# Kernel optimization log

Hardware: AMD Instinct MI355X
Metric: run time of the kernel (lower is better)

Reference implementation:

```python
import jax, jax.numpy as jnp
import numpy as np

HIDDEN = 1024
FFN = 4096
N_EXPERTS = 8
TOP_K = 2


def setup_inputs() -> dict:
    key = jax.random.key(0)
    ks = jax.random.split(key, 6)
    x = jax.random.normal(ks[0], (2, 2048, HIDDEN), dtype=jnp.float32)
    Wr = jax.random.normal(ks[1], (N_EXPERTS, HIDDEN), dtype=jnp.float32) * 0.02
    W1 = jax.random.normal(ks[2], (N_EXPERTS, FFN, HIDDEN), dtype=jnp.float32) * 0.02
    b1 = jnp.zeros((N_EXPERTS, FFN), dtype=jnp.float32)
    W2 = jax.random.normal(ks[3], (N_EXPERTS, HIDDEN, FFN), dtype=jnp.float32) * 0.02
    b2 = jnp.zeros((N_EXPERTS, HIDDEN), dtype=jnp.float32)
    return {"x": x, "Wr": Wr, "W1": W1, "b1": b1, "W2": W2, "b2": b2}


def reference(x, Wr, W1, b1, W2, b2):
    # x: [B, S, D]; Wr: [E, D]; W1: [E, F, D]; W2: [E, D, F]
    B, S, D = x.shape
    E = Wr.shape[0]
    xf = x.reshape(-1, D)                              # [T, D]
    T = xf.shape[0]
    logits = xf @ Wr.T                                 # [T, E]
    probs = jax.nn.softmax(logits, axis=-1)
    top_v, top_i = jax.lax.top_k(probs, TOP_K)         # [T, K]
    top_v = top_v / jnp.sum(top_v, axis=-1, keepdims=True)
    # combine weights: zero except the top-k experts per token
    comb = jnp.zeros((T, E), dtype=xf.dtype).at[jnp.arange(T)[:, None], top_i].add(top_v)
    # run every expert densely (same math as gather/FFN/weighted-scatter)
    h = jax.nn.gelu(jnp.einsum('td,efd->etf', xf, W1) + b1[:, None, :], approximate=False)  # [E, T, F]
    y = jnp.einsum('etf,edf->etd', h, W2) + b2[:, None, :]                                   # [E, T, D]
    out = jnp.einsum('etd,te->td', y, comb)            # weighted combine
    return out.reshape(B, S, D)
```

## Files before the change

kernel.cpp:

```cpp
#include <hip/hip_runtime.h>

#define HIDDEN 1024
#define FFN    4096
#define NEXP   8
#define TOKENS 4096
#define ASSIGN 8192

typedef __attribute__((ext_vector_type(8))) short s8v;
typedef __attribute__((ext_vector_type(4))) float f4v;

__device__ __forceinline__ float bf2f(ushort u) {
    return __uint_as_float(((unsigned int)u) << 16);
}
__device__ __forceinline__ ushort f2bf(float f) {
    unsigned int x = __float_as_uint(f);
    return (ushort)((x + 0x7fffu + ((x >> 16) & 1u)) >> 16);
}

#define GLDS16(g, l) __builtin_amdgcn_global_load_lds( \
    (const __attribute__((address_space(1))) unsigned int*)(g), \
    (__attribute__((address_space(3))) unsigned int*)(l), 16, 0, 0)

__global__ void conv_kernel(const float4* __restrict__ src, ushort4* __restrict__ dst) {
    const int i = blockIdx.x * blockDim.x + threadIdx.x;
    const float4 v = src[i];
    ushort4 o;
    o.x = f2bf(v.x); o.y = f2bf(v.y); o.z = f2bf(v.z); o.w = f2bf(v.w);
    dst[i] = o;
}

__global__ void router_kernel(const float* __restrict__ x, const float* __restrict__ Wr,
                              int* __restrict__ counts, int* __restrict__ topk_idx,
                              float* __restrict__ topk_w) {
    const int tok  = blockIdx.x;
    const int lane = threadIdx.x;
    float acc[NEXP];
#pragma unroll
    for (int e = 0; e < NEXP; ++e) acc[e] = 0.f;
#pragma unroll
    for (int i = 0; i < HIDDEN / 64; ++i) {
        const int idx = i * 64 + lane;
        const float xv = x[(size_t)tok * HIDDEN + idx];
#pragma unroll
        for (int e = 0; e < NEXP; ++e) acc[e] += xv * Wr[e * HIDDEN + idx];
    }
#pragma unroll
    for (int e = 0; e < NEXP; ++e) {
#pragma unroll
        for (int off = 32; off > 0; off >>= 1) acc[e] += __shfl_xor(acc[e], off);
    }
    if (lane == 0) {
        int i0 = 0;
        for (int e = 1; e < NEXP; ++e) if (acc[e] > acc[i0]) i0 = e;
        int i1 = (i0 == 0) ? 1 : 0;
        for (int e = 0; e < NEXP; ++e) if (e != i0 && acc[e] > acc[i1]) i1 = e;
        const float e1 = expf(acc[i1] - acc[i0]);
        const float s  = 1.f + e1;
        topk_idx[tok * 2 + 0] = i0;
        topk_idx[tok * 2 + 1] = i1;
        topk_w[tok * 2 + 0]   = 1.f / s;
        topk_w[tok * 2 + 1]   = e1 / s;
        atomicAdd(&counts[i0], 1);
        atomicAdd(&counts[i1], 1);
    }
}

__global__ void prefix_kernel(const int* __restrict__ counts, int* __restrict__ offsets,
                              int* __restrict__ cursors) {
    if (threadIdx.x == 0) {
        int s = 0;
        for (int e = 0; e < NEXP; ++e) { offsets[e] = s; cursors[e] = s; s += counts[e]; }
        offsets[NEXP] = s;
    }
}

__global__ void scatter_kernel(const int* __restrict__ topk_idx, const float* __restrict__ topk_w,
                               int* __restrict__ cursors, int* __restrict__ token_list,
                               float* __restrict__ weight_list, int* __restrict__ slot_of) {
    const int a = blockIdx.x * blockDim.x + threadIdx.x;
    if (a >= ASSIGN) return;
    const int e   = topk_idx[a];
    const int pos = atomicAdd(&cursors[e], 1);
    token_list[pos]  = a >> 1;
    weight_list[pos] = topk_w[a];
    slot_of[a]       = pos;
}

__global__ __launch_bounds__(256)
void gemm1_kernel(const ushort* __restrict__ x, const ushort* __restrict__ W1,
                  const float* __restrict__ b1, const int* __restrict__ token_list,
                  const int* __restrict__ counts, const int* __restrict__ offsets,
                  ushort* __restrict__ h) {
    const int e      = blockIdx.z;
    const int n_e    = counts[e];
    const int tile_m = blockIdx.y;
    if (n_e <= 0 || tile_m * 128 >= n_e) return;
    const int tile_n = blockIdx.x;
    const int base   = offsets[e];

    __shared__ __align__(16) ushort As[128 * 32];
    __shared__ __align__(16) ushort Bs[128 * 32];

    const int t    = threadIdx.x;
    const int lane = t & 63;
    const int wv   = t >> 6;
    const int srow = t >> 2;
    const int scol = (t & 3) * 8;

    const int r0 = tile_m * 128 + srow;
    const int r1 = r0 + 64;
    const int tokA0 = token_list[base + (r0 < n_e ? r0 : n_e - 1)];
    const int tokA1 = token_list[base + (r1 < n_e ? r1 : n_e - 1)];
    const ushort* gA0 = x + (size_t)tokA0 * HIDDEN + scol;
    const ushort* gA1 = x + (size_t)tokA1 * HIDDEN + scol;
    const ushort* gB0 = W1 + ((size_t)e * FFN + tile_n * 128 + srow) * HIDDEN + scol;
    const ushort* gB1 = W1 + ((size_t)e * FFN + tile_n * 128 + 64 + srow) * HIDDEN + scol;

    ushort* lA0 = As + wv * 512;
    ushort* lA1 = As + 2048 + wv * 512;
    ushort* lB0 = Bs + wv * 512;
    ushort* lB1 = Bs + 2048 + wv * 512;

    f4v acc[4][4];
#pragma unroll
    for (int i = 0; i < 4; ++i)
#pragma unroll
        for (int j = 0; j < 4; ++j) { f4v z = {0.f, 0.f, 0.f, 0.f}; acc[i][j] = z; }

    const int row_off = (wv & 1) * 64;
    const int col_off = (wv >> 1) * 64;
    const int l15 = lane & 15;
    const int lq  = lane >> 4;

    for (int k0 = 0; k0 < HIDDEN; k0 += 32) {
        GLDS16(gA0 + k0, lA0);
        GLDS16(gA1 + k0, lA1);
        GLDS16(gB0 + k0, lB0);
        GLDS16(gB1 + k0, lB1);
        __syncthreads();
        s8v a[4], b[4];
#pragma unroll
        for (int i = 0; i < 4; ++i) a[i] = *(const s8v*)(As + (row_off + i * 16 + l15) * 32 + lq * 8);
#pragma unroll
        for (int j = 0; j < 4; ++j) b[j] = *(const s8v*)(Bs + (col_off + j * 16 + l15) * 32 + lq * 8);
#pragma unroll
        for (int i = 0; i < 4; ++i)
#pragma unroll
            for (int j = 0; j < 4; ++j)
                acc[i][j] = __builtin_amdgcn_mfma_f32_16x16x32_bf16(a[i], b[j], acc[i][j], 0, 0, 0);
        __syncthreads();
    }

    const int mrem = n_e - tile_m * 128;
#pragma unroll
    for (int i = 0; i < 4; ++i) {
#pragma unroll
        for (int r = 0; r < 4; ++r) {
            const int m_loc = row_off + i * 16 + lq * 4 + r;
            if (m_loc < mrem) {
                const size_t hrow = (size_t)(base + tile_m * 128 + m_loc) * FFN;
#pragma unroll
                for (int j = 0; j < 4; ++j) {
                    const int colF = tile_n * 128 + col_off + j * 16 + l15;
                    float v = acc[i][j][r] + b1[e * FFN + colF];
                    v = 0.5f * v * (1.0f + erff(v * 0.70710678118654752f));
                    h[hrow + colF] = f2bf(v);
                }
            }
        }
    }
}

__global__ __launch_bounds__(256)
void gemm2_kernel(const ushort* __restrict__ h, const ushort* __restrict__ W2,
                  const float* __restrict__ b2, const float* __restrict__ weight_list,
                  const int* __restrict__ counts, const int* __restrict__ offsets,
                  ushort* __restrict__ y) {
    const int e      = blockIdx.z;
    const int n_e    = counts[e];
    const int tile_m = blockIdx.y;
    if (n_e <= 0 || tile_m * 128 >= n_e) return;
    const int tile_n = blockIdx.x;
    const int base   = offsets[e];

    __shared__ __align__(16) ushort As[128 * 32];
    __shared__ __align__(16) ushort Bs[128 * 32];

    const int t    = threadIdx.x;
    const int lane = t & 63;
    const int wv   = t >> 6;
    const int srow = t >> 2;
    const int scol = (t & 3) * 8;

    const int r0 = tile_m * 128 + srow;
    const int r1 = r0 + 64;
    const int slot0 = base + (r0 < n_e ? r0 : n_e - 1);
    const int slot1 = base + (r1 < n_e ? r1 : n_e - 1);
    const ushort* gA0 = h + (size_t)slot0 * FFN + scol;
    const ushort* gA1 = h + (size_t)slot1 * FFN + scol;
    const ushort* gB0 = W2 + ((size_t)e * HIDDEN + tile_n * 128 + srow) * FFN + scol;
    const ushort* gB1 = W2 + ((size_t)e * HIDDEN + tile_n * 128 + 64 + srow) * FFN + scol;

    ushort* lA0 = As + wv * 512;
    ushort* lA1 = As + 2048 + wv * 512;
    ushort* lB0 = Bs + wv * 512;
    ushort* lB1 = Bs + 2048 + wv * 512;

    f4v acc[4][4];
#pragma unroll
    for (int i = 0; i < 4; ++i)
#pragma unroll
        for (int j = 0; j < 4; ++j) { f4v z = {0.f, 0.f, 0.f, 0.f}; acc[i][j] = z; }

    const int row_off = (wv & 1) * 64;
    const int col_off = (wv >> 1) * 64;
    const int l15 = lane & 15;
    const int lq  = lane >> 4;

    for (int k0 = 0; k0 < FFN; k0 += 32) {
        GLDS16(gA0 + k0, lA0);
        GLDS16(gA1 + k0, lA1);
        GLDS16(gB0 + k0, lB0);
        GLDS16(gB1 + k0, lB1);
        __syncthreads();
        s8v a[4], b[4];
#pragma unroll
        for (int i = 0; i < 4; ++i) a[i] = *(const s8v*)(As + (row_off + i * 16 + l15) * 32 + lq * 8);
#pragma unroll
        for (int j = 0; j < 4; ++j) b[j] = *(const s8v*)(Bs + (col_off + j * 16 + l15) * 32 + lq * 8);
#pragma unroll
        for (int i = 0; i < 4; ++i)
#pragma unroll
            for (int j = 0; j < 4; ++j)
                acc[i][j] = __builtin_amdgcn_mfma_f32_16x16x32_bf16(a[i], b[j], acc[i][j], 0, 0, 0);
        __syncthreads();
    }

    const int mrem = n_e - tile_m * 128;
#pragma unroll
    for (int i = 0; i < 4; ++i) {
#pragma unroll
        for (int r = 0; r < 4; ++r) {
            const int m_loc = row_off + i * 16 + lq * 4 + r;
            if (m_loc < mrem) {
                const int slot = base + tile_m * 128 + m_loc;
                const float wgt = weight_list[slot];
#pragma unroll
                for (int j = 0; j < 4; ++j) {
                    const int colD = tile_n * 128 + col_off + j * 16 + l15;
                    const float v = acc[i][j][r] + b2[e * HIDDEN + colD];
                    y[(size_t)slot * HIDDEN + colD] = f2bf(v * wgt);
                }
            }
        }
    }
}

__global__ void combine_kernel(const int* __restrict__ slot_of, const ushort* __restrict__ y,
                               float* __restrict__ out) {
    const int idx = blockIdx.x * blockDim.x + threadIdx.x;
    const int t = idx >> 8;
    const int d = (idx & 255) * 4;
    const int s0 = slot_of[t * 2 + 0];
    const int s1 = slot_of[t * 2 + 1];
    const ushort4 a = *(const ushort4*)(y + (size_t)s0 * HIDDEN + d);
    const ushort4 b = *(const ushort4*)(y + (size_t)s1 * HIDDEN + d);
    float4 o;
    o.x = bf2f(a.x) + bf2f(b.x);
    o.y = bf2f(a.y) + bf2f(b.y);
    o.z = bf2f(a.z) + bf2f(b.z);
    o.w = bf2f(a.w) + bf2f(b.w);
    *(float4*)(out + (size_t)t * HIDDEN + d) = o;
}

extern "C" void kernel_launch(void* const* d_in, const int* in_sizes, int n_in,
                              void* d_out, int out_size, void* d_ws, size_t ws_size,
                              hipStream_t stream) {
    const float* x  = (const float*)d_in[0];
    const float* Wr = (const float*)d_in[1];
    const float* W1 = (const float*)d_in[2];
    const float* b1 = (const float*)d_in[3];
    const float* W2 = (const float*)d_in[4];
    const float* b2 = (const float*)d_in[5];
    float* out = (float*)d_out;

    char* ws = (char*)d_ws;
    int*    counts      = (int*)(ws + 0);
    int*    offsets     = (int*)(ws + 256);
    int*    cursors     = (int*)(ws + 512);
    int*    topk_idx    = (int*)(ws + 1024);
    float*  topk_w      = (float*)(ws + 1024 + 32768);
    int*    slot_of     = (int*)(ws + 1024 + 65536);
    int*    token_list  = (int*)(ws + 1024 + 98304);
    float*  weight_list = (float*)(ws + 1024 + 131072);
    ushort* x_bf        = (ushort*)(ws + (1 << 20));
    ushort* wbuf        = (ushort*)(ws + (1 << 20) + 8388608);
    ushort* h           = (ushort*)(ws + (1 << 20) + 8388608 + 67108864);
    ushort* y           = (ushort*)(ws + (1 << 20) + 8388608 + 2 * 67108864ull);

    const int NW = NEXP * FFN * HIDDEN;

    hipMemsetAsync(counts, 0, 64, stream);
    conv_kernel<<<(TOKENS * HIDDEN / 4) / 256, 256, 0, stream>>>((const float4*)x, (ushort4*)x_bf);
    conv_kernel<<<(NW / 4) / 256, 256, 0, stream>>>((const float4*)W1, (ushort4*)wbuf);

    router_kernel<<<TOKENS, 64, 0, stream>>>(x, Wr, counts, topk_idx, topk_w);
    prefix_kernel<<<1, 64, 0, stream>>>(counts, offsets, cursors);
    scatter_kernel<<<ASSIGN / 256, 256, 0, stream>>>(topk_idx, topk_w, cursors,
                                                     token_list, weight_list, slot_of);

    gemm1_kernel<<<dim3(FFN / 128, ASSIGN / 128, NEXP), 256, 0, stream>>>(
        x_bf, wbuf, b1, token_list, counts, offsets, h);

    conv_kernel<<<(NW / 4) / 256, 256, 0, stream>>>((const float4*)W2, (ushort4*)wbuf);

    gemm2_kernel<<<dim3(HIDDEN / 128, ASSIGN / 128, NEXP), 256, 0, stream>>>(
        h, wbuf, b2, weight_list, counts, offsets, y);

    combine_kernel<<<(TOKENS * HIDDEN / 4) / 256, 256, 0, stream>>>(slot_of, y, out);
}
```

Before: 694.5 us.

## Swizzle LDS tiles, interleave expert block order, narrow gemm2 N-tile

Adds an XOR swizzle to the LDS layout of the A and B tiles, applied both to where global_load_lds writes and to where the MFMA operands are read, to reduce bank conflicts. Flattens the grid into one dimension with the expert index in the low bits, so consecutive blocks are spread across experts and early-exiting blocks are interleaved. Gemm2's N tile is halved to 64 so more blocks are in flight for its K=4096 loop, at the cost of reading each A tile from global memory twice as often.

```diff
diff --git a/kernel.cpp b/kernel.cpp
--- a/kernel.cpp
+++ b/kernel.cpp
@@ -20,6 +20,14 @@
 #define GLDS16(g, l) __builtin_amdgcn_global_load_lds( \
     (const __attribute__((address_space(1))) unsigned int*)(g), \
     (__attribute__((address_space(3))) unsigned int*)(l), 16, 0, 0)
+
+__device__ __forceinline__ int swz_scol(int t) {
+    const int srow = t >> 2, c = t & 3;
+    return ((c ^ ((srow >> 1) & 3)) << 3);
+}
+__device__ __forceinline__ int lds_off(int row, int lq) {
+    return row * 32 + ((lq ^ ((row >> 1) & 3)) << 3);
+}
 
 __global__ void conv_kernel(const float4* __restrict__ src, ushort4* __restrict__ dst) {
     const int i = blockIdx.x * blockDim.x + threadIdx.x;
@@ -91,11 +99,13 @@
                   const float* __restrict__ b1, const int* __restrict__ token_list,
                   const int* __restrict__ counts, const int* __restrict__ offsets,
                   ushort* __restrict__ h) {
-    const int e      = blockIdx.z;
+    const int bid    = blockIdx.x;
+    const int e      = bid & 7;
+    const int r      = bid >> 3;
+    const int tile_m = r & 63;
+    const int tile_n = r >> 6;
     const int n_e    = counts[e];
-    const int tile_m = blockIdx.y;
     if (n_e <= 0 || tile_m * 128 >= n_e) return;
-    const int tile_n = blockIdx.x;
     const int base   = offsets[e];
 
     __shared__ __align__(16) ushort As[128 * 32];
@@ -105,7 +115,7 @@
     const int lane = t & 63;
     const int wv   = t >> 6;
     const int srow = t >> 2;
-    const int scol = (t & 3) * 8;
+    const int scol = swz_scol(t);
 
     const int r0 = tile_m * 128 + srow;
     const int r1 = r0 + 64;
@@ -140,9 +150,9 @@
         __syncthreads();
         s8v a[4], b[4];
 #pragma unroll
-        for (int i = 0; i < 4; ++i) a[i] = *(const s8v*)(As + (row_off + i * 16 + l15) * 32 + lq * 8);
-#pragma unroll
-        for (int j = 0; j < 4; ++j) b[j] = *(const s8v*)(Bs + (col_off + j * 16 + l15) * 32 + lq * 8);
+        for (int i = 0; i < 4; ++i) a[i] = *(const s8v*)(As + lds_off(row_off + i * 16 + l15, lq));
+#pragma unroll
+        for (int j = 0; j < 4; ++j) b[j] = *(const s8v*)(Bs + lds_off(col_off + j * 16 + l15, lq));
 #pragma unroll
         for (int i = 0; i < 4; ++i)
 #pragma unroll
@@ -155,14 +165,14 @@
 #pragma unroll
     for (int i = 0; i < 4; ++i) {
 #pragma unroll
-        for (int r = 0; r < 4; ++r) {
-            const int m_loc = row_off + i * 16 + lq * 4 + r;
+        for (int rr = 0; rr < 4; ++rr) {
+            const int m_loc = row_off + i * 16 + lq * 4 + rr;
             if (m_loc < mrem) {
                 const size_t hrow = (size_t)(base + tile_m * 128 + m_loc) * FFN;
 #pragma unroll
                 for (int j = 0; j < 4; ++j) {
                     const int colF = tile_n * 128 + col_off + j * 16 + l15;
-                    float v = acc[i][j][r] + b1[e * FFN + colF];
+                    float v = acc[i][j][rr] + b1[e * FFN + colF];
                     v = 0.5f * v * (1.0f + erff(v * 0.70710678118654752f));
                     h[hrow + colF] = f2bf(v);
                 }
@@ -176,21 +186,23 @@
                   const float* __restrict__ b2, const float* __restrict__ weight_list,
                   const int* __restrict__ counts, const int* __restrict__ offsets,
                   ushort* __restrict__ y) {
-    const int e      = blockIdx.z;
+    const int bid    = blockIdx.x;
+    const int e      = bid & 7;
+    const int r      = bid >> 3;
+    const int tile_m = r & 63;
+    const int tile_n = r >> 6;
     const int n_e    = counts[e];
-    const int tile_m = blockIdx.y;
     if (n_e <= 0 || tile_m * 128 >= n_e) return;
-    const int tile_n = blockIdx.x;
     const int base   = offsets[e];
 
     __shared__ __align__(16) ushort As[128 * 32];
-    __shared__ __align__(16) ushort Bs[128 * 32];
+    __shared__ __align__(16) ushort Bs[64 * 32];
 
     const int t    = threadIdx.x;
     const int lane = t & 63;
     const int wv   = t >> 6;
     const int srow = t >> 2;
-    const int scol = (t & 3) * 8;
+    const int scol = swz_scol(t);
 
     const int r0 = tile_m * 128 + srow;
     const int r1 = r0 + 64;
@@ -198,40 +210,37 @@
     const int slot1 = base + (r1 < n_e ? r1 : n_e - 1);
     const ushort* gA0 = h + (size_t)slot0 * FFN + scol;
     const ushort* gA1 = h + (size_t)slot1 * FFN + scol;
-    const ushort* gB0 = W2 + ((size_t)e * HIDDEN + tile_n * 128 + srow) * FFN + scol;
-    const ushort* gB1 = W2 + ((size_t)e * HIDDEN + tile_n * 128 + 64 + srow) * FFN + scol;
+    const ushort* gB  = W2 + ((size_t)e * HIDDEN + tile_n * 64 + srow) * FFN + scol;
 
     ushort* lA0 = As + wv * 512;
     ushort* lA1 = As + 2048 + wv * 512;
-    ushort* lB0 = Bs + wv * 512;
-    ushort* lB1 = Bs + 2048 + wv * 512;
-
-    f4v acc[4][4];
+    ushort* lB  = Bs + wv * 512;
+
+    f4v acc[4][2];
 #pragma unroll
     for (int i = 0; i < 4; ++i)
 #pragma unroll
-        for (int j = 0; j < 4; ++j) { f4v z = {0.f, 0.f, 0.f, 0.f}; acc[i][j] = z; }
+        for (int j = 0; j < 2; ++j) { f4v z = {0.f, 0.f, 0.f, 0.f}; acc[i][j] = z; }
 
     const int row_off = (wv & 1) * 64;
-    const int col_off = (wv >> 1) * 64;
+    const int col_off = (wv >> 1) * 32;
     const int l15 = lane & 15;
     const int lq  = lane >> 4;
 
     for (int k0 = 0; k0 < FFN; k0 += 32) {
         GLDS16(gA0 + k0, lA0);
         GLDS16(gA1 + k0, lA1);
-        GLDS16(gB0 + k0, lB0);
-        GLDS16(gB1 + k0, lB1);
+        GLDS16(gB  + k0, lB);
         __syncthreads();
-        s8v a[4], b[4];
-#pragma unroll
-        for (int i = 0; i < 4; ++i) a[i] = *(const s8v*)(As + (row_off + i * 16 + l15) * 32 + lq * 8);
-#pragma unroll
-        for (int j = 0; j < 4; ++j) b[j] = *(const s8v*)(Bs + (col_off + j * 16 + l15) * 32 + lq * 8);
+        s8v a[4], b[2];
+#pragma unroll
+        for (int i = 0; i < 4; ++i) a[i] = *(const s8v*)(As + lds_off(row_off + i * 16 + l15, lq));
+#pragma unroll
+        for (int j = 0; j < 2; ++j) b[j] = *(const s8v*)(Bs + lds_off(col_off + j * 16 + l15, lq));
 #pragma unroll
         for (int i = 0; i < 4; ++i)
 #pragma unroll
-            for (int j = 0; j < 4; ++j)
+            for (int j = 0; j < 2; ++j)
                 acc[i][j] = __builtin_amdgcn_mfma_f32_16x16x32_bf16(a[i], b[j], acc[i][j], 0, 0, 0);
         __syncthreads();
     }
@@ -240,15 +249,15 @@
 #pragma unroll
     for (int i = 0; i < 4; ++i) {
 #pragma unroll
-        for (int r = 0; r < 4; ++r) {
-            const int m_loc = row_off + i * 16 + lq * 4 + r;
+        for (int rr = 0; rr < 4; ++rr) {
+            const int m_loc = row_off + i * 16 + lq * 4 + rr;
             if (m_loc < mrem) {
                 const int slot = base + tile_m * 128 + m_loc;
                 const float wgt = weight_list[slot];
 #pragma unroll
-                for (int j = 0; j < 4; ++j) {
-                    const int colD = tile_n * 128 + col_off + j * 16 + l15;
-                    const float v = acc[i][j][r] + b2[e * HIDDEN + colD];
+                for (int j = 0; j < 2; ++j) {
+                    const int colD = tile_n * 64 + col_off + j * 16 + l15;
+                    const float v = acc[i][j][rr] + b2[e * HIDDEN + colD];
                     y[(size_t)slot * HIDDEN + colD] = f2bf(v * wgt);
                 }
             }
@@ -309,12 +318,12 @@
     scatter_kernel<<<ASSIGN / 256, 256, 0, stream>>>(topk_idx, topk_w, cursors,
                                                      token_list, weight_list, slot_of);
 
-    gemm1_kernel<<<dim3(FFN / 128, ASSIGN / 128, NEXP), 256, 0, stream>>>(
+    gemm1_kernel<<<NEXP * 64 * (FFN / 128), 256, 0, stream>>>(
         x_bf, wbuf, b1, token_list, counts, offsets, h);
 
     conv_kernel<<<(NW / 4) / 256, 256, 0, stream>>>((const float4*)W2, (ushort4*)wbuf);
 
-    gemm2_kernel<<<dim3(HIDDEN / 128, ASSIGN / 128, NEXP), 256, 0, stream>>>(
+    gemm2_kernel<<<NEXP * 64 * (HIDDEN / 64), 256, 0, stream>>>(
         h, wbuf, b2, weight_list, counts, offsets, y);
 
     combine_kernel<<<(TOKENS * HIDDEN / 4) / 256, 256, 0, stream>>>(slot_of, y, out);
```

Result: slower. 749.1 us (+7.9%).
